# Kernel optimization log

Measured on AMD Instinct MI355X. Metric: run time of the kernel, lower is better.

## Reference

```python
import jax, jax.numpy as jnp
import numpy as np

EPS = 1e-6  # torch F.cosine_similarity eps


def setup_inputs() -> dict:
    key = jax.random.key(0)
    k1, k2, k3, k4, k5 = jax.random.split(key, 5)
    N, D, E = 100000, 256, 500000
    z_drug = jax.random.normal(k1, (N, D), dtype=jnp.float32)
    z_adr = jax.random.normal(k2, (N, D), dtype=jnp.float32)
    w = jax.random.normal(k3, (1, 1), dtype=jnp.float32)
    b = jax.random.normal(k4, (1,), dtype=jnp.float32)
    edge_index = jax.random.randint(k5, (2, E), 0, N, dtype=jnp.int64)
    return {"z_drug": z_drug, "z_adr": z_adr, "w": w, "b": b,
            "edge_index": edge_index, "type_id": 1}


def reference(z_drug, z_adr, w, b, edge_index, type_id):
    # type_id==1 branch: cosine_similarity(z_drug[row_0], z_adr[row_1]);
    # all other branches are the identical pattern on other table pairs.
    row_0, row_1 = edge_index[0], edge_index[1]
    x = z_drug[row_0]  # [E, D] gather
    y = z_adr[row_1]   # [E, D] gather
    # torch semantics: dot / (max(||x||, eps) * max(||y||, eps))
    nx = jnp.maximum(jnp.sqrt(jnp.sum(x * x, axis=-1)), EPS)
    ny = jnp.maximum(jnp.sqrt(jnp.sum(y * y, axis=-1)), EPS)
    sim = jnp.sum(x * y, axis=-1) / (nx * ny)  # [E]
    # apply_linear=True: Linear(1,1) on sim.view(-1,1), then squeeze
    return sim * w[0, 0] + b[0]
```

## Files before the change

### kernel.cpp

```cpp
#include <hip/hip_runtime.h>


#define EPS 1e-6f

__device__ __forceinline__ int sdot4(int a, int b, int c) {
#if __has_builtin(__builtin_amdgcn_sdot4)
    return __builtin_amdgcn_sdot4(a, b, c, false);
#else
    #pragma unroll
    for (int i = 0; i < 4; ++i)
        c += ((a << (24 - 8 * i)) >> 24) * ((b << (24 - 8 * i)) >> 24);
    return c;
#endif
}

__global__ __launch_bounds__(256) void quant_rows_kernel(
    const float* __restrict__ in, unsigned int* __restrict__ out, int nRows)
{
    const int wave = (blockIdx.x * blockDim.x + threadIdx.x) >> 6;
    const int lane = threadIdx.x & 63;
    if (wave >= nRows) return;

    const float4 v = reinterpret_cast<const float4*>(in + (size_t)wave * 256)[lane];

    float amax = fmaxf(fmaxf(fabsf(v.x), fabsf(v.y)), fmaxf(fabsf(v.z), fabsf(v.w)));
    #pragma unroll
    for (int off = 32; off >= 1; off >>= 1)
        amax = fmaxf(amax, __shfl_xor(amax, off, 64));

    const float s = amax > 0.f ? 127.f / amax : 0.f;
    const int q0 = (int)__builtin_rintf(v.x * s);
    const int q1 = (int)__builtin_rintf(v.y * s);
    const int q2 = (int)__builtin_rintf(v.z * s);
    const int q3 = (int)__builtin_rintf(v.w * s);
    const unsigned int packed = (q0 & 0xFF) | ((q1 & 0xFF) << 8) |
                                ((q2 & 0xFF) << 16) | ((q3 & 0xFF) << 24);
    out[(size_t)wave * 64 + lane] = packed;
}

__global__ __launch_bounds__(256) void edge_cosine_i8_kernel(
    const unsigned int* __restrict__ zx,
    const unsigned int* __restrict__ zy,
    const float* __restrict__ w,
    const float* __restrict__ b,
    const int* __restrict__ edge_index,
    float* __restrict__ out,
    int E)
{
    const int tid  = blockIdx.x * blockDim.x + threadIdx.x;
    const int edge = tid >> 4;
    const int sub  = threadIdx.x & 15;
    if (edge >= E) return;

    const int r0 = edge_index[edge];
    const int r1 = edge_index[E + edge];

    const int4 x = reinterpret_cast<const int4*>(zx + (size_t)r0 * 64)[sub];
    const int4 y = reinterpret_cast<const int4*>(zy + (size_t)r1 * 64)[sub];

    int dxy = 0, dxx = 0, dyy = 0;
    dxy = sdot4(x.x, y.x, dxy); dxx = sdot4(x.x, x.x, dxx); dyy = sdot4(y.x, y.x, dyy);
    dxy = sdot4(x.y, y.y, dxy); dxx = sdot4(x.y, x.y, dxx); dyy = sdot4(y.y, y.y, dyy);
    dxy = sdot4(x.z, y.z, dxy); dxx = sdot4(x.z, x.z, dxx); dyy = sdot4(y.z, y.z, dyy);
    dxy = sdot4(x.w, y.w, dxy); dxx = sdot4(x.w, x.w, dxx); dyy = sdot4(y.w, y.w, dyy);

    #pragma unroll
    for (int off = 8; off >= 1; off >>= 1) {
        dxy += __shfl_xor(dxy, off, 64);
        dxx += __shfl_xor(dxx, off, 64);
        dyy += __shfl_xor(dyy, off, 64);
    }

    if (sub == 0) {
        const float nx = fmaxf(sqrtf((float)dxx), EPS);
        const float ny = fmaxf(sqrtf((float)dyy), EPS);
        const float sim = (float)dxy / (nx * ny);
        out[edge] = sim * w[0] + b[0];
    }
}

__global__ __launch_bounds__(256) void edge_cosine_f32_kernel(
    const float* __restrict__ z_drug,
    const float* __restrict__ z_adr,
    const float* __restrict__ w,
    const float* __restrict__ b,
    const int* __restrict__ edge_index,
    float* __restrict__ out,
    int E)
{
    const int tid  = blockIdx.x * blockDim.x + threadIdx.x;
    const int edge = tid >> 4;
    const int sub  = threadIdx.x & 15;
    if (edge >= E) return;

    const int r0 = edge_index[edge];
    const int r1 = edge_index[E + edge];

    const float4* xp = reinterpret_cast<const float4*>(z_drug + (size_t)r0 * 256);
    const float4* yp = reinterpret_cast<const float4*>(z_adr  + (size_t)r1 * 256);

    const float4 x0 = xp[sub +  0], x1 = xp[sub + 16], x2 = xp[sub + 32], x3 = xp[sub + 48];
    const float4 y0 = yp[sub +  0], y1 = yp[sub + 16], y2 = yp[sub + 32], y3 = yp[sub + 48];

    float dxy, dxx, dyy;
    dxy  = x0.x * y0.x + x0.y * y0.y + x0.z * y0.z + x0.w * y0.w;
    dxy += x1.x * y1.x + x1.y * y1.y + x1.z * y1.z + x1.w * y1.w;
    dxy += x2.x * y2.x + x2.y * y2.y + x2.z * y2.z + x2.w * y2.w;
    dxy += x3.x * y3.x + x3.y * y3.y + x3.z * y3.z + x3.w * y3.w;
    dxx  = x0.x * x0.x + x0.y * x0.y + x0.z * x0.z + x0.w * x0.w;
    dxx += x1.x * x1.x + x1.y * x1.y + x1.z * x1.z + x1.w * x1.w;
    dxx += x2.x * x2.x + x2.y * x2.y + x2.z * x2.z + x2.w * x2.w;
    dxx += x3.x * x3.x + x3.y * x3.y + x3.z * x3.z + x3.w * x3.w;
    dyy  = y0.x * y0.x + y0.y * y0.y + y0.z * y0.z + y0.w * y0.w;
    dyy += y1.x * y1.x + y1.y * y1.y + y1.z * y1.z + y1.w * y1.w;
    dyy += y2.x * y2.x + y2.y * y2.y + y2.z * y2.z + y2.w * y2.w;
    dyy += y3.x * y3.x + y3.y * y3.y + y3.z * y3.z + y3.w * y3.w;

    #pragma unroll
    for (int off = 8; off >= 1; off >>= 1) {
        dxy += __shfl_xor(dxy, off, 64);
        dxx += __shfl_xor(dxx, off, 64);
        dyy += __shfl_xor(dyy, off, 64);
    }

    if (sub == 0) {
        const float nx = fmaxf(sqrtf(dxx), EPS);
        const float ny = fmaxf(sqrtf(dyy), EPS);
        const float sim = dxy / (nx * ny);
        out[edge] = sim * w[0] + b[0];
    }
}

extern "C" void kernel_launch(void* const* d_in, const int* in_sizes, int n_in,
                              void* d_out, int out_size, void* d_ws, size_t ws_size,
                              hipStream_t stream)
{
    const float* z_drug = (const float*)d_in[0];
    const float* z_adr  = (const float*)d_in[1];
    const float* w      = (const float*)d_in[2];
    const float* b      = (const float*)d_in[3];
    const int*   ei     = (const int*)d_in[4];

    float* out = (float*)d_out;
    const int E  = in_sizes[4] / 2;
    const int nD = in_sizes[0];
    const int nA = in_sizes[1];
    const int rowsD = nD / 256;
    const int rowsA = nA / 256;

    const size_t needWs = (size_t)nD + (size_t)nA;

    const int block = 256;
    const int edgesPerBlock = block / 16;
    const int egrid = (E + edgesPerBlock - 1) / edgesPerBlock;

    if (ws_size >= needWs) {
        unsigned int* qx = (unsigned int*)d_ws;
        unsigned int* qy = qx + (size_t)rowsD * 64;

        const int rowsPerBlock = block / 64;
        quant_rows_kernel<<<(rowsD + rowsPerBlock - 1) / rowsPerBlock, block, 0, stream>>>(
            z_drug, qx, rowsD);
        quant_rows_kernel<<<(rowsA + rowsPerBlock - 1) / rowsPerBlock, block, 0, stream>>>(
            z_adr, qy, rowsA);

        edge_cosine_i8_kernel<<<egrid, block, 0, stream>>>(qx, qy, w, b, ei, out, E);
    } else {
        edge_cosine_f32_kernel<<<egrid, block, 0, stream>>>(z_drug, z_adr, w, b, ei, out, E);
    }
}
```

Measured before the change: 80.45 us.

## Bucket-sort edges by source row and fuse both quantization passes into one kernel

Both embedding tables are now quantized in a single launch, using nontemporal loads. A histogram, scan and scatter pass then bucket the edges by the high bits of the source row, and the int8 cosine kernel reads these sorted (r0, r1, idx) records and writes each result back to its original position. The goal is more cache reuse of source rows during the gather. In exchange it adds several launches, a memset, global atomics contending on a few hundred cursors, an extra 16-byte-per-edge buffer, and scattered output writes.

After: 281.7 us. +250.1%, slower.

```diff
diff --git a/kernel.cpp b/kernel.cpp
--- a/kernel.cpp
+++ b/kernel.cpp
@@ -2,6 +2,8 @@
 
 
 #define EPS 1e-6f
+
+typedef float f32x4 __attribute__((ext_vector_type(4)));
 
 __device__ __forceinline__ int sdot4(int a, int b, int c) {
 #if __has_builtin(__builtin_amdgcn_sdot4)
@@ -14,14 +16,21 @@
 #endif
 }
 
-__global__ __launch_bounds__(256) void quant_rows_kernel(
-    const float* __restrict__ in, unsigned int* __restrict__ out, int nRows)
+__global__ __launch_bounds__(256) void quant_rows2_kernel(
+    const float* __restrict__ zd, const float* __restrict__ za,
+    unsigned int* __restrict__ qx, unsigned int* __restrict__ qy,
+    int rowsD, int rowsTotal)
 {
     const int wave = (blockIdx.x * blockDim.x + threadIdx.x) >> 6;
     const int lane = threadIdx.x & 63;
-    if (wave >= nRows) return;
-
-    const float4 v = reinterpret_cast<const float4*>(in + (size_t)wave * 256)[lane];
+    if (wave >= rowsTotal) return;
+
+    const float* src; unsigned int* dst; int row;
+    if (wave < rowsD) { src = zd; dst = qx; row = wave; }
+    else              { src = za; dst = qy; row = wave - rowsD; }
+
+    const f32x4* p = reinterpret_cast<const f32x4*>(src + (size_t)row * 256);
+    const f32x4 v = __builtin_nontemporal_load(&p[lane]);
 
     float amax = fmaxf(fmaxf(fabsf(v.x), fabsf(v.y)), fmaxf(fabsf(v.z), fabsf(v.w)));
     #pragma unroll
@@ -35,15 +44,59 @@
     const int q3 = (int)__builtin_rintf(v.w * s);
     const unsigned int packed = (q0 & 0xFF) | ((q1 & 0xFF) << 8) |
                                 ((q2 & 0xFF) << 16) | ((q3 & 0xFF) << 24);
-    out[(size_t)wave * 64 + lane] = packed;
-}
-
-__global__ __launch_bounds__(256) void edge_cosine_i8_kernel(
-    const unsigned int* __restrict__ zx,
-    const unsigned int* __restrict__ zy,
+    dst[(size_t)row * 64 + lane] = packed;
+}
+
+__global__ __launch_bounds__(256) void hist_kernel(
+    const int* __restrict__ ei, int E, int nB, int shift,
+    unsigned int* __restrict__ hist)
+{
+    __shared__ unsigned int lh[1024];
+    for (int i = threadIdx.x; i < nB; i += 256) lh[i] = 0;
+    __syncthreads();
+    for (int i = blockIdx.x * 256 + threadIdx.x; i < E; i += gridDim.x * 256)
+        atomicAdd(&lh[((unsigned)ei[i]) >> shift], 1u);
+    __syncthreads();
+    for (int i = threadIdx.x; i < nB; i += 256)
+        if (lh[i]) atomicAdd(&hist[i], lh[i]);
+}
+
+__global__ __launch_bounds__(1024) void scan_kernel(
+    const unsigned int* __restrict__ hist, unsigned int* __restrict__ cursor, int nB)
+{
+    __shared__ unsigned int tmp[1024];
+    const int t = threadIdx.x;
+    const unsigned int v = (t < nB) ? hist[t] : 0u;
+    tmp[t] = v;
+    __syncthreads();
+    #pragma unroll
+    for (int off = 1; off < 1024; off <<= 1) {
+        const unsigned int add = (t >= off) ? tmp[t - off] : 0u;
+        __syncthreads();
+        tmp[t] += add;
+        __syncthreads();
+    }
+    if (t < nB) cursor[t] = tmp[t] - v;
+}
+
+__global__ __launch_bounds__(256) void scatter_kernel(
+    const int* __restrict__ ei, int E, int shift,
+    unsigned int* __restrict__ cursor, int4* __restrict__ rre)
+{
+    const int i = blockIdx.x * 256 + threadIdx.x;
+    if (i >= E) return;
+    const int r0 = ei[i];
+    const int r1 = ei[E + i];
+    const unsigned int pos = atomicAdd(&cursor[((unsigned)r0) >> shift], 1u);
+    rre[pos] = make_int4(r0, r1, i, 0);
+}
+
+__global__ __launch_bounds__(256) void edge_cosine_i8_sorted_kernel(
+    const unsigned int* __restrict__ qx,
+    const unsigned int* __restrict__ qy,
     const float* __restrict__ w,
     const float* __restrict__ b,
-    const int* __restrict__ edge_index,
+    const int4* __restrict__ rre,
     float* __restrict__ out,
     int E)
 {
@@ -52,11 +105,10 @@
     const int sub  = threadIdx.x & 15;
     if (edge >= E) return;
 
-    const int r0 = edge_index[edge];
-    const int r1 = edge_index[E + edge];
-
-    const int4 x = reinterpret_cast<const int4*>(zx + (size_t)r0 * 64)[sub];
-    const int4 y = reinterpret_cast<const int4*>(zy + (size_t)r1 * 64)[sub];
+    const int4 rec = rre[edge];
+
+    const int4 x = reinterpret_cast<const int4*>(qx + (size_t)rec.x * 64)[sub];
+    const int4 y = reinterpret_cast<const int4*>(qy + (size_t)rec.y * 64)[sub];
 
     int dxy = 0, dxx = 0, dyy = 0;
     dxy = sdot4(x.x, y.x, dxy); dxx = sdot4(x.x, x.x, dxx); dyy = sdot4(y.x, y.x, dyy);
@@ -75,7 +127,7 @@
         const float nx = fmaxf(sqrtf((float)dxx), EPS);
         const float ny = fmaxf(sqrtf((float)dyy), EPS);
         const float sim = (float)dxy / (nx * ny);
-        out[edge] = sim * w[0] + b[0];
+        out[rec.z] = sim * w[0] + b[0];
     }
 }
 
@@ -148,23 +200,38 @@
     const int rowsD = nD / 256;
     const int rowsA = nA / 256;
 
-    const size_t needWs = (size_t)nD + (size_t)nA;
+    int shift = 8;
+    while (((rowsD - 1) >> shift) + 1 > 1024) ++shift;
+    const int nB = ((rowsD - 1) >> shift) + 1;
+
+    const size_t qxBytes   = (size_t)rowsD * 256;
+    const size_t qyBytes   = (size_t)rowsA * 256;
+    const size_t histBytes = 1024 * sizeof(unsigned int);
+    const size_t needWs    = qxBytes + qyBytes + 2 * histBytes + (size_t)E * 16;
 
     const int block = 256;
     const int edgesPerBlock = block / 16;
     const int egrid = (E + edgesPerBlock - 1) / edgesPerBlock;
 
     if (ws_size >= needWs) {
-        unsigned int* qx = (unsigned int*)d_ws;
-        unsigned int* qy = qx + (size_t)rowsD * 64;
-
+        char* p = (char*)d_ws;
+        unsigned int* qx     = (unsigned int*)p;              p += qxBytes;
+        unsigned int* qy     = (unsigned int*)p;              p += qyBytes;
+        unsigned int* hist   = (unsigned int*)p;              p += histBytes;
+        unsigned int* cursor = (unsigned int*)p;              p += histBytes;
+        int4*         rre    = (int4*)p;
+
+        const int rowsTotal = rowsD + rowsA;
         const int rowsPerBlock = block / 64;
-        quant_rows_kernel<<<(rowsD + rowsPerBlock - 1) / rowsPerBlock, block, 0, stream>>>(
-            z_drug, qx, rowsD);
-        quant_rows_kernel<<<(rowsA + rowsPerBlock - 1) / rowsPerBlock, block, 0, stream>>>(
-            z_adr, qy, rowsA);
-
-        edge_cosine_i8_kernel<<<egrid, block, 0, stream>>>(qx, qy, w, b, ei, out, E);
+        quant_rows2_kernel<<<(rowsTotal + rowsPerBlock - 1) / rowsPerBlock, block, 0, stream>>>(
+            z_drug, z_adr, qx, qy, rowsD, rowsTotal);
+
+        (void)hipMemsetAsync(hist, 0, histBytes, stream);
+        hist_kernel<<<512, block, 0, stream>>>(ei, E, nB, shift, hist);
+        scan_kernel<<<1, 1024, 0, stream>>>(hist, cursor, nB);
+        scatter_kernel<<<(E + block - 1) / block, block, 0, stream>>>(ei, E, shift, cursor, rre);
+
+        edge_cosine_i8_sorted_kernel<<<egrid, block, 0, stream>>>(qx, qy, w, b, rre, out, E);
     } else {
         edge_cosine_f32_kernel<<<egrid, block, 0, stream>>>(z_drug, z_adr, w, b, ei, out, E);
     }
```

## Fuse row quantization, precompute inverse norms, use 4 lanes per edge

Applied to the files above, without the earlier changes.

Merges the two per-table quantization launches into one kernel and uses nontemporal loads for the fp32 tables. The quantization kernel now also computes each row's inverse quantized norm, so the edge kernel needs only the cross dot product. The edge kernel assigns 4 lanes per edge instead of 16, so each lane does four int4 loads and fewer shuffle reductions are needed. This cuts dot4 work and launch overhead, at the cost of two extra scattered scalar loads per edge and lower memory-level parallelism per edge.

Result: slower. 96.22 us (+19.6%).

```diff
diff --git a/kernel.cpp b/kernel.cpp
--- a/kernel.cpp
+++ b/kernel.cpp
@@ -2,6 +2,8 @@
 
 
 #define EPS 1e-6f
+
+typedef float f32x4 __attribute__((ext_vector_type(4)));
 
 __device__ __forceinline__ int sdot4(int a, int b, int c) {
 #if __has_builtin(__builtin_amdgcn_sdot4)
@@ -14,14 +16,22 @@
 #endif
 }
 
-__global__ __launch_bounds__(256) void quant_rows_kernel(
-    const float* __restrict__ in, unsigned int* __restrict__ out, int nRows)
+__global__ __launch_bounds__(256) void quant_rows2_kernel(
+    const float* __restrict__ zd, const float* __restrict__ za,
+    unsigned int* __restrict__ qx, unsigned int* __restrict__ qy,
+    float* __restrict__ invx, float* __restrict__ invy,
+    int rowsD, int rowsTotal)
 {
     const int wave = (blockIdx.x * blockDim.x + threadIdx.x) >> 6;
     const int lane = threadIdx.x & 63;
-    if (wave >= nRows) return;
+    if (wave >= rowsTotal) return;
 
-    const float4 v = reinterpret_cast<const float4*>(in + (size_t)wave * 256)[lane];
+    const float* src; unsigned int* dst; float* inv; int row;
+    if (wave < rowsD) { src = zd; dst = qx; inv = invx; row = wave; }
+    else              { src = za; dst = qy; inv = invy; row = wave - rowsD; }
+
+    const f32x4* p = reinterpret_cast<const f32x4*>(src + (size_t)row * 256);
+    const f32x4 v = __builtin_nontemporal_load(&p[lane]);
 
     float amax = fmaxf(fmaxf(fabsf(v.x), fabsf(v.y)), fmaxf(fabsf(v.z), fabsf(v.w)));
     #pragma unroll
@@ -35,12 +45,22 @@
     const int q3 = (int)__builtin_rintf(v.w * s);
     const unsigned int packed = (q0 & 0xFF) | ((q1 & 0xFF) << 8) |
                                 ((q2 & 0xFF) << 16) | ((q3 & 0xFF) << 24);
-    out[(size_t)wave * 64 + lane] = packed;
+    dst[(size_t)row * 64 + lane] = packed;
+
+    int ssq = q0 * q0 + q1 * q1 + q2 * q2 + q3 * q3;
+    #pragma unroll
+    for (int off = 32; off >= 1; off >>= 1)
+        ssq += __shfl_xor(ssq, off, 64);
+
+    if (lane == 0)
+        inv[row] = 1.0f / fmaxf(sqrtf((float)ssq), EPS);
 }
 
 __global__ __launch_bounds__(256) void edge_cosine_i8_kernel(
-    const unsigned int* __restrict__ zx,
-    const unsigned int* __restrict__ zy,
+    const unsigned int* __restrict__ qx,
+    const unsigned int* __restrict__ qy,
+    const float* __restrict__ invx,
+    const float* __restrict__ invy,
     const float* __restrict__ w,
     const float* __restrict__ b,
     const int* __restrict__ edge_index,
@@ -48,33 +68,34 @@
     int E)
 {
     const int tid  = blockIdx.x * blockDim.x + threadIdx.x;
-    const int edge = tid >> 4;
-    const int sub  = threadIdx.x & 15;
+    const int edge = tid >> 2;
+    const int sub  = threadIdx.x & 3;
     if (edge >= E) return;
 
     const int r0 = edge_index[edge];
     const int r1 = edge_index[E + edge];
 
-    const int4 x = reinterpret_cast<const int4*>(zx + (size_t)r0 * 64)[sub];
-    const int4 y = reinterpret_cast<const int4*>(zy + (size_t)r1 * 64)[sub];
+    const int4* xp = reinterpret_cast<const int4*>(qx + (size_t)r0 * 64);
+    const int4* yp = reinterpret_cast<const int4*>(qy + (size_t)r1 * 64);
 
-    int dxy = 0, dxx = 0, dyy = 0;
-    dxy = sdot4(x.x, y.x, dxy); dxx = sdot4(x.x, x.x, dxx); dyy = sdot4(y.x, y.x, dyy);
-    dxy = sdot4(x.y, y.y, dxy); dxx = sdot4(x.y, x.y, dxx); dyy = sdot4(y.y, y.y, dyy);
-    dxy = sdot4(x.z, y.z, dxy); dxx = sdot4(x.z, x.z, dxx); dyy = sdot4(y.z, y.z, dyy);
-    dxy = sdot4(x.w, y.w, dxy); dxx = sdot4(x.w, x.w, dxx); dyy = sdot4(y.w, y.w, dyy);
+    const int4 x0 = xp[sub], x1 = xp[sub + 4], x2 = xp[sub + 8], x3 = xp[sub + 12];
+    const int4 y0 = yp[sub], y1 = yp[sub + 4], y2 = yp[sub + 8], y3 = yp[sub + 12];
 
-    #pragma unroll
-    for (int off = 8; off >= 1; off >>= 1) {
-        dxy += __shfl_xor(dxy, off, 64);
-        dxx += __shfl_xor(dxx, off, 64);
-        dyy += __shfl_xor(dyy, off, 64);
-    }
+    int dxy = 0;
+    dxy = sdot4(x0.x, y0.x, dxy); dxy = sdot4(x0.y, y0.y, dxy);
+    dxy = sdot4(x0.z, y0.z, dxy); dxy = sdot4(x0.w, y0.w, dxy);
+    dxy = sdot4(x1.x, y1.x, dxy); dxy = sdot4(x1.y, y1.y, dxy);
+    dxy = sdot4(x1.z, y1.z, dxy); dxy = sdot4(x1.w, y1.w, dxy);
+    dxy = sdot4(x2.x, y2.x, dxy); dxy = sdot4(x2.y, y2.y, dxy);
+    dxy = sdot4(x2.z, y2.z, dxy); dxy = sdot4(x2.w, y2.w, dxy);
+    dxy = sdot4(x3.x, y3.x, dxy); dxy = sdot4(x3.y, y3.y, dxy);
+    dxy = sdot4(x3.z, y3.z, dxy); dxy = sdot4(x3.w, y3.w, dxy);
+
+    dxy += __shfl_xor(dxy, 2, 64);
+    dxy += __shfl_xor(dxy, 1, 64);
 
     if (sub == 0) {
-        const float nx = fmaxf(sqrtf((float)dxx), EPS);
-        const float ny = fmaxf(sqrtf((float)dyy), EPS);
-        const float sim = (float)dxy / (nx * ny);
+        const float sim = (float)dxy * invx[r0] * invy[r1];
         out[edge] = sim * w[0] + b[0];
     }
 }
@@ -148,24 +169,31 @@
     const int rowsD = nD / 256;
     const int rowsA = nA / 256;
 
-    const size_t needWs = (size_t)nD + (size_t)nA;
+    const size_t qxBytes = (size_t)rowsD * 256;
+    const size_t qyBytes = (size_t)rowsA * 256;
+    const size_t needWs  = qxBytes + qyBytes + (size_t)(rowsD + rowsA) * sizeof(float);
 
     const int block = 256;
-    const int edgesPerBlock = block / 16;
-    const int egrid = (E + edgesPerBlock - 1) / edgesPerBlock;
 
     if (ws_size >= needWs) {
-        unsigned int* qx = (unsigned int*)d_ws;
-        unsigned int* qy = qx + (size_t)rowsD * 64;
+        char* p = (char*)d_ws;
+        unsigned int* qx   = (unsigned int*)p;   p += qxBytes;
+        unsigned int* qy   = (unsigned int*)p;   p += qyBytes;
+        float*        invx = (float*)p;          p += (size_t)rowsD * sizeof(float);
+        float*        invy = (float*)p;
 
+        const int rowsTotal = rowsD + rowsA;
         const int rowsPerBlock = block / 64;
-        quant_rows_kernel<<<(rowsD + rowsPerBlock - 1) / rowsPerBlock, block, 0, stream>>>(
-            z_drug, qx, rowsD);
-        quant_rows_kernel<<<(rowsA + rowsPerBlock - 1) / rowsPerBlock, block, 0, stream>>>(
-            z_adr, qy, rowsA);
+        quant_rows2_kernel<<<(rowsTotal + rowsPerBlock - 1) / rowsPerBlock, block, 0, stream>>>(
+            z_drug, z_adr, qx, qy, invx, invy, rowsD, rowsTotal);
 
-        edge_cosine_i8_kernel<<<egrid, block, 0, stream>>>(qx, qy, w, b, ei, out, E);
+        const int edgesPerBlock = block / 4;
+        const int egrid = (E + edgesPerBlock - 1) / edgesPerBlock;
+        edge_cosine_i8_kernel<<<egrid, block, 0, stream>>>(
+            qx, qy, invx, invy, w, b, ei, out, E);
     } else {
+        const int edgesPerBlock = block / 16;
+        const int egrid = (E + edgesPerBlock - 1) / edgesPerBlock;
         edge_cosine_f32_kernel<<<egrid, block, 0, stream>>>(z_drug, z_adr, w, b, ei, out, E);
     }
 }
```
